# Optimization experiments

Measured on AMD Instinct MI355X. Metric: run time of the kernel, lower is better.

Reference implementation:

```python
import jax, jax.numpy as jnp
import numpy as np

B, T, C = 4, 2048, 1024
NH = 16
HD = C // NH  # 64


def setup_inputs() -> dict:
    key = jax.random.key(0)
    k1, k2, k3 = jax.random.split(key, 3)
    x = jax.random.normal(k1, (B, T, C), dtype=jnp.float32)
    # causal mask buffer, 1 = keep, 0 = mask out
    mask = jnp.tril(jnp.ones((T, T), dtype=jnp.int32))[None, None, :, :]
    # learned params (Linear with bias=False): torch stores weight as [out, in],
    # y = x @ W.T ; we store transposed for direct matmul
    w_qkv = jax.random.normal(k2, (C, 3 * C), dtype=jnp.float32) / np.sqrt(C)
    w_proj = jax.random.normal(k3, (C, C), dtype=jnp.float32) / np.sqrt(C)
    return {"x": x, "mask": mask, "w_qkv": w_qkv, "w_proj": w_proj}


def reference(x, mask, w_qkv, w_proj):
    b, t, c = x.shape
    qkv = x @ w_qkv  # [b, t, 3c]
    q, k, v = jnp.split(qkv, 3, axis=-1)
    # [b, nh, t, hd]
    q = q.reshape(b, t, NH, HD).transpose(0, 2, 1, 3)
    k = k.reshape(b, t, NH, HD).transpose(0, 2, 1, 3)
    v = v.reshape(b, t, NH, HD).transpose(0, 2, 1, 3)
    att = jnp.einsum("bhqd,bhkd->bhqk", q, k) * (1.0 / np.sqrt(HD))
    att = jnp.where(mask == 0, -jnp.inf, att)
    att = jax.nn.softmax(att, axis=-1)
    y = jnp.einsum("bhqk,bhkd->bhqd", att, v)
    y = y.transpose(0, 2, 1, 3).reshape(b, t, c)
    return y @ w_proj
```

## Files before the change

### kernel.cpp

```cpp
#include <hip/hip_runtime.h>
#include <hip/hip_bf16.h>

typedef _Float16 f16;
typedef __attribute__((ext_vector_type(4))) _Float16 f16x4;
typedef __attribute__((ext_vector_type(8))) _Float16 f16x8;
typedef __attribute__((ext_vector_type(4))) float f32x4;

#define MFMA16(a, b, c) __builtin_amdgcn_mfma_f32_16x16x16f16((a), (b), (c), 0, 0, 0)
#define MFMA32(a, b, c) __builtin_amdgcn_mfma_f32_16x16x32_f16((a), (b), (c), 0, 0, 0)
#define EXP2(x) __builtin_amdgcn_exp2f(x)
#define GLOAD_LDS16(g, l)                                                        \
  __builtin_amdgcn_global_load_lds((const __attribute__((address_space(1))) void*)(g), \
                                   (__attribute__((address_space(3))) void*)(l), 16, 0, 0)
typedef const __attribute__((address_space(3))) char* lds_cp;
#define TR16(dst, addr, imm) \
  asm volatile("ds_read_b64_tr_b16 %0, %1 offset:" imm : "=v"(dst) : "v"(addr))

__device__ __forceinline__ float max3f(float a, float b, float c) {
  return fmaxf(fmaxf(a, b), c);
}

__global__ __launch_bounds__(256) void prep_kernel(
    const float* __restrict__ x, f16* __restrict__ x16,
    const float* __restrict__ wq, f16* __restrict__ wqT,
    const float* __restrict__ wp, f16* __restrict__ wpT) {
  const int blk = blockIdx.x;
  const int tid = threadIdx.x;
  if (blk < 8192) {
    int i = blk * 256 + tid;
    const float4 v = reinterpret_cast<const float4*>(x)[i];
    f16x4 h;
    h[0] = (f16)v.x; h[1] = (f16)v.y; h[2] = (f16)v.z; h[3] = (f16)v.w;
    reinterpret_cast<f16x4*>(x16)[i] = h;
    return;
  }
  const float* src;
  f16* dst;
  int R, Cc, bx, by;
  if (blk < 11264) {
    int j = blk - 8192;
    bx = j % 96; by = j / 96;
    src = wq; dst = wqT; R = 1024; Cc = 3072;
  } else {
    int j = blk - 11264;
    bx = j & 31; by = j >> 5;
    src = wp; dst = wpT; R = 1024; Cc = 1024;
  }
  __shared__ float t[32][33];
  int tx0 = bx * 32, ty0 = by * 32;
  int c = tid & 31;
  int r0 = tid >> 5;
#pragma unroll
  for (int i = 0; i < 4; i++) {
    int r = r0 + 8 * i;
    t[r][c] = src[(size_t)(ty0 + r) * Cc + tx0 + c];
  }
  __syncthreads();
#pragma unroll
  for (int i = 0; i < 4; i++) {
    int a = r0 + 8 * i;
    dst[(size_t)(tx0 + a) * R + ty0 + c] = (f16)t[c][a];
  }
}

__global__ __launch_bounds__(512, 2) void gemm_qkv_kernel(
    const f16* __restrict__ A, const f16* __restrict__ Bt, f16* __restrict__ C,
    int M, int N, int K) {
  __shared__ __align__(16) char smem[114688];
  const int tid = threadIdx.x;
  const int lane = tid & 63, wid = tid >> 6;
  const int wm = wid >> 2, wn = wid & 3;
  const int lo = lane & 15, hi = lane >> 4;

  const int ntn = N / 192;
  const int nwg = (M >> 8) * ntn;
  const int wg = (blockIdx.x & 7) * (nwg >> 3) + (blockIdx.x >> 3);
  const int tm0 = (wg / ntn) << 8;
  const int tn0 = (wg % ntn) * 192;

  const int prow = tid >> 3;
  const int u8 = (tid & 7) ^ (prow & 7);
  const f16* asrc[4];
  const f16* bsrc[3];
#pragma unroll
  for (int c = 0; c < 4; c++) asrc[c] = A + (size_t)(tm0 + c * 64 + prow) * K + u8 * 8;
#pragma unroll
  for (int c = 0; c < 3; c++) bsrc[c] = Bt + (size_t)(tn0 + c * 64 + prow) * K + u8 * 8;

  const int swz = lo & 7;
  const int s0 = (hi ^ swz) << 4, s1 = ((4 + hi) ^ swz) << 4;
  const int aoff0 = wm * 16384 + lo * 128 + s0;
  const int aoff1 = wm * 16384 + lo * 128 + s1;
  int boff0[3], boff1[3];
#pragma unroll
  for (int ni = 0; ni < 3; ni++) {
    int cr = 3 * wn + ni;
    int base = 32768 + (cr >> 2) * 8192 + ((cr & 3) * 16 + lo) * 128;
    boff0[ni] = base + s0;
    boff1[ni] = base + s1;
  }

  f32x4 acc[8][3] = {};

  auto stageA = [&](int kt, char* buf) {
#pragma unroll
    for (int c = 0; c < 4; c++)
      GLOAD_LDS16(asrc[c] + kt, buf + c * 8192 + tid * 16);
  };
  auto stageB = [&](int kt, char* buf) {
#pragma unroll
    for (int c = 0; c < 3; c++)
      GLOAD_LDS16(bsrc[c] + kt, buf + 32768 + c * 8192 + tid * 16);
  };

  const int NT = K >> 6;
  stageA(0, smem);
  stageB(0, smem);

  for (int t = 0; t < NT; t++) {
    char* db = smem + (t & 1) * 57344;
    char* nb = smem + ((t + 1) & 1) * 57344;
    const int kt1 = (t + 1) << 6;

    asm volatile("s_waitcnt vmcnt(0)" ::: "memory");
    __builtin_amdgcn_s_barrier();
    f16x8 a[4][2], b[3][2];
#pragma unroll
    for (int mi = 0; mi < 4; mi++) {
      a[mi][0] = *(const f16x8*)(db + aoff0 + mi * 2048);
      a[mi][1] = *(const f16x8*)(db + aoff1 + mi * 2048);
    }
#pragma unroll
    for (int ni = 0; ni < 3; ni++) {
      b[ni][0] = *(const f16x8*)(db + boff0[ni]);
      b[ni][1] = *(const f16x8*)(db + boff1[ni]);
    }
    if (t + 1 < NT) stageA(kt1, nb);
    asm volatile("s_waitcnt lgkmcnt(0)" ::: "memory");
    __builtin_amdgcn_sched_barrier(0);
    __builtin_amdgcn_s_setprio(1);
#pragma unroll
    for (int mi = 0; mi < 4; mi++)
#pragma unroll
      for (int ni = 0; ni < 3; ni++) {
        acc[mi][ni] = MFMA32(a[mi][0], b[ni][0], acc[mi][ni]);
        acc[mi][ni] = MFMA32(a[mi][1], b[ni][1], acc[mi][ni]);
      }
    __builtin_amdgcn_s_setprio(0);

    __builtin_amdgcn_s_barrier();
#pragma unroll
    for (int mi = 0; mi < 4; mi++) {
      a[mi][0] = *(const f16x8*)(db + aoff0 + 8192 + mi * 2048);
      a[mi][1] = *(const f16x8*)(db + aoff1 + 8192 + mi * 2048);
    }
    if (t + 1 < NT) stageB(kt1, nb);
    asm volatile("s_waitcnt lgkmcnt(0)" ::: "memory");
    __builtin_amdgcn_sched_barrier(0);
    __builtin_amdgcn_s_setprio(1);
#pragma unroll
    for (int mi = 0; mi < 4; mi++)
#pragma unroll
      for (int ni = 0; ni < 3; ni++) {
        acc[4 + mi][ni] = MFMA32(a[mi][0], b[ni][0], acc[4 + mi][ni]);
        acc[4 + mi][ni] = MFMA32(a[mi][1], b[ni][1], acc[4 + mi][ni]);
      }
    __builtin_amdgcn_s_setprio(0);
  }

#pragma unroll
  for (int mi = 0; mi < 8; mi++)
#pragma unroll
    for (int ni = 0; ni < 3; ni++)
#pragma unroll
      for (int r = 0; r < 4; r++) {
        int row = tm0 + wm * 128 + mi * 16 + 4 * hi + r;
        int col = tn0 + wn * 48 + ni * 16 + lo;
        C[(size_t)row * N + col] = (f16)acc[mi][ni][r];
      }
}

template <bool OUT_F32>
__global__ __launch_bounds__(256) void gemm_f16_kernel(
    const f16* __restrict__ A, const f16* __restrict__ Bt, void* __restrict__ Cout,
    int M, int N, int K) {
  constexpr int BK = 32;
  __shared__ f16 Al[3][128 * BK];
  __shared__ f16 Bl[3][128 * BK];

  const int tid = threadIdx.x;
  const int lane = tid & 63, wid = tid >> 6;
  const int wm = wid >> 1, wn = wid & 1;
  const int lo = lane & 15, hi = lane >> 4;
  const int tn0 = blockIdx.x * 128, tm0 = blockIdx.y * 128;

  f32x4 acc[4][4] = {};

  const int r1 = tid >> 2, o1 = (tid & 3) * 8;

  auto stage = [&](int kt, int c) {
    GLOAD_LDS16(&A[(size_t)(tm0 + r1) * K + kt + o1], &Al[c][tid * 8]);
    GLOAD_LDS16(&A[(size_t)(tm0 + r1 + 64) * K + kt + o1], &Al[c][(tid + 256) * 8]);
    GLOAD_LDS16(&Bt[(size_t)(tn0 + r1) * K + kt + o1], &Bl[c][tid * 8]);
    GLOAD_LDS16(&Bt[(size_t)(tn0 + r1 + 64) * K + kt + o1], &Bl[c][(tid + 256) * 8]);
  };

  auto compute = [&](int cur) {
    f16x8 af[4], bf[4];
#pragma unroll
    for (int mi = 0; mi < 4; mi++)
      af[mi] = *(const f16x8*)&Al[cur][(wm * 64 + mi * 16 + lo) * BK + 8 * hi];
#pragma unroll
    for (int ni = 0; ni < 4; ni++)
      bf[ni] = *(const f16x8*)&Bl[cur][(wn * 64 + ni * 16 + lo) * BK + 8 * hi];
    __builtin_amdgcn_s_setprio(1);
#pragma unroll
    for (int mi = 0; mi < 4; mi++)
#pragma unroll
      for (int ni = 0; ni < 4; ni++)
        acc[mi][ni] = MFMA32(af[mi], bf[ni], acc[mi][ni]);
    __builtin_amdgcn_s_setprio(0);
  };

  const int NT = K / BK;
  stage(0, 0);
  stage(BK, 1);

  int cur = 0;
  for (int t = 0; t < NT - 1; t++) {
    asm volatile("s_waitcnt vmcnt(4)" ::: "memory");
    __builtin_amdgcn_s_barrier();
    if (t + 2 < NT) stage((t + 2) * BK, (t + 2) % 3);
    compute(cur);
    cur = (cur == 2) ? 0 : cur + 1;
  }
  asm volatile("s_waitcnt vmcnt(0)" ::: "memory");
  __builtin_amdgcn_s_barrier();
  compute(cur);

#pragma unroll
  for (int mi = 0; mi < 4; mi++)
#pragma unroll
    for (int ni = 0; ni < 4; ni++)
#pragma unroll
      for (int r = 0; r < 4; r++) {
        int row = tm0 + wm * 64 + mi * 16 + 4 * hi + r;
        int col = tn0 + wn * 64 + ni * 16 + lo;
        float v = acc[mi][ni][r];
        if (OUT_F32)
          ((float*)Cout)[(size_t)row * N + col] = v;
        else
          ((f16*)Cout)[(size_t)row * N + col] = (f16)v;
      }
}

__global__ __launch_bounds__(256, 4) void attn_kernel(
    const f16* __restrict__ qkv, f16* __restrict__ y) {
  constexpr int T = 2048, NHD = 3072, LDO = 72;
  const int bh = blockIdx.x;
  const int b = bh >> 4, h = bh & 15;
  const int pr = blockIdx.y;
  const int tid = threadIdx.x;
  const int lane = tid & 63, w = tid >> 6;
  const int lo = lane & 15, hi = lane >> 4;

  const size_t base = (size_t)b * T * NHD + (size_t)h * 64;
  const f16* Qp = qkv + base;
  const f16* Kp = qkv + base + 1024;
  const f16* Vp = qkv + base + 2048;

  __shared__ __align__(16) char smem[32768];
  f16 (*Ol)[LDO] = (f16(*)[LDO])smem;

  const int tile[2] = {pr, 31 - pr};
  const int qb[2] = {tile[0] * 64 + w * 16, tile[1] * 64 + w * 16};

  const float scf = 0.125f * 1.44269504089f;
  f16x8 qf[2][2];
#pragma unroll
  for (int s = 0; s < 2; s++) {
    const f16* qrow = Qp + (size_t)(qb[s] + lo) * NHD;
#pragma unroll
    for (int ks = 0; ks < 2; ks++) {
      f16x8 v = *(const f16x8*)&qrow[ks * 32 + 8 * hi];
#pragma unroll
      for (int j = 0; j < 8; j++) v[j] = (f16)((float)v[j] * scf);
      qf[s][ks] = v;
    }
  }

  f32x4 oacc[2][4] = {};
  f32x4 lacc[2] = {};
  float mreg[2] = {-1e30f, -1e30f};
  const f16x4 ones4 = {(f16)1.f, (f16)1.f, (f16)1.f, (f16)1.f};

  const int kr = tid >> 3;
  const int kslot = (tid & 7) ^ (kr & 7);
  const int tp = tid & 127;
  const int vkey = 4 * (tp >> 3) + ((tp >> 1) & 3);
  const int vcol = (tid >> 7) * 16 + (tid & 1) * 8;

  const int kfo0 = lo * 64 + ((hi ^ (lo & 7)) * 8);
  const int kfo1 = lo * 64 + (((4 + hi) ^ (lo & 7)) * 8);

  auto stage = [&](int kv, int c) {
    char* kb = smem + c * 8192;
    char* vb = smem + 16384 + c * 8192;
    GLOAD_LDS16(&Kp[(size_t)(kv + kr) * NHD + kslot * 8], kb + tid * 16);
    GLOAD_LDS16(&Kp[(size_t)(kv + kr + 32) * NHD + kslot * 8], kb + 4096 + tid * 16);
    GLOAD_LDS16(&Vp[(size_t)(kv + vkey) * NHD + vcol], vb + tid * 16);
    GLOAD_LDS16(&Vp[(size_t)(kv + vkey) * NHD + vcol + 32], vb + 4096 + tid * 16);
  };

  const int nt = 32 - pr;
  stage(0, 0);
  asm volatile("s_waitcnt vmcnt(0)" ::: "memory");
  __builtin_amdgcn_s_barrier();

  for (int t = 0; t < nt; t++) {
    const int cur = t & 1;
    const int kv0 = t * 64;
    if (t + 1 < nt) stage(kv0 + 64, cur ^ 1);

    const f16* Kl = (const f16*)(smem + cur * 8192);
    const bool act0 = kv0 <= qb[0] + 15;

    f16x8 kf[2][4];
#pragma unroll
    for (int ct = 0; ct < 4; ct++) {
      kf[0][ct] = *(const f16x8*)&Kl[ct * 1024 + kfo0];
      kf[1][ct] = *(const f16x8*)&Kl[ct * 1024 + kfo1];
    }

    f16x4 pb[2][4];
#pragma unroll
    for (int s = 0; s < 2; s++) {
      if (s == 0 && !act0) continue;
      f32x4 s_[4] = {};
      __builtin_amdgcn_s_setprio(1);
#pragma unroll
      for (int ks = 0; ks < 2; ks++)
#pragma unroll
        for (int ct = 0; ct < 4; ct++)
          s_[ct] = MFMA32(kf[ks][ct], qf[s][ks], s_[ct]);
      __builtin_amdgcn_s_setprio(0);

      if (kv0 + 63 > qb[s]) {
        const int q = qb[s] + lo;
#pragma unroll
        for (int ct = 0; ct < 4; ct++)
#pragma unroll
          for (int r = 0; r < 4; r++)
            if (kv0 + ct * 16 + 4 * hi + r > q) s_[ct][r] = -3.0e38f;
      }
      float t0 = max3f(s_[0][0], s_[0][1], s_[0][2]);
      float t1 = max3f(s_[0][3], s_[1][0], s_[1][1]);
      float t2 = max3f(s_[1][2], s_[1][3], s_[2][0]);
      float t3 = max3f(s_[2][1], s_[2][2], s_[2][3]);
      float t4 = max3f(s_[3][0], s_[3][1], s_[3][2]);
      float mt = fmaxf(max3f(t0, t1, t2), max3f(t3, t4, s_[3][3]));
      mt = fmaxf(mt, __shfl_xor(mt, 16));
      mt = fmaxf(mt, __shfl_xor(mt, 32));
      float mn = mreg[s];
      if (!__all(mt <= mn + 8.f)) {
        mn = fmaxf(mn, mt);
        const float al = EXP2(mreg[s] - mn);
        mreg[s] = mn;
#pragma unroll
        for (int r = 0; r < 4; r++) lacc[s][r] *= al;
#pragma unroll
        for (int ct = 0; ct < 4; ct++)
#pragma unroll
          for (int r = 0; r < 4; r++) oacc[s][ct][r] *= al;
      }
#pragma unroll
      for (int ct = 0; ct < 4; ct++)
#pragma unroll
        for (int r = 0; r < 4; r++)
          pb[s][ct][r] = (f16)EXP2(s_[ct][r] - mn);
      __builtin_amdgcn_s_setprio(1);
#pragma unroll
      for (int kk = 0; kk < 4; kk++)
        lacc[s] = MFMA16(ones4, pb[s][kk], lacc[s]);
      __builtin_amdgcn_s_setprio(0);
    }

    lds_cp vtrb = (lds_cp)(smem + 16384 + cur * 8192) + lane * 8;
#pragma unroll
    for (int ct = 0; ct < 4; ct++) {
      lds_cp bct = vtrb + ct * 2048;
      f16x4 v0, v1, v2, v3;
      TR16(v0, bct, "0");
      TR16(v1, bct, "512");
      TR16(v2, bct, "1024");
      TR16(v3, bct, "1536");
      asm volatile("s_waitcnt lgkmcnt(0)" ::: "memory");
      __builtin_amdgcn_sched_barrier(0);
      __builtin_amdgcn_s_setprio(1);
      if (act0) {
        oacc[0][ct] = MFMA16(v0, pb[0][0], oacc[0][ct]);
        oacc[0][ct] = MFMA16(v1, pb[0][1], oacc[0][ct]);
        oacc[0][ct] = MFMA16(v2, pb[0][2], oacc[0][ct]);
        oacc[0][ct] = MFMA16(v3, pb[0][3], oacc[0][ct]);
      }
      oacc[1][ct] = MFMA16(v0, pb[1][0], oacc[1][ct]);
      oacc[1][ct] = MFMA16(v1, pb[1][1], oacc[1][ct]);
      oacc[1][ct] = MFMA16(v2, pb[1][2], oacc[1][ct]);
      oacc[1][ct] = MFMA16(v3, pb[1][3], oacc[1][ct]);
      __builtin_amdgcn_s_setprio(0);
    }

    asm volatile("s_waitcnt vmcnt(0)" ::: "memory");
    __builtin_amdgcn_s_barrier();
  }

#pragma unroll
  for (int s = 0; s < 2; s++) {
    __syncthreads();
    const float inv = 1.f / lacc[s][0];
#pragma unroll
    for (int ct = 0; ct < 4; ct++) {
      f16x4 o4;
#pragma unroll
      for (int r = 0; r < 4; r++) o4[r] = (f16)(oacc[s][ct][r] * inv);
      *(f16x4*)&Ol[w * 16 + lo][ct * 16 + 4 * hi] = o4;
    }
    __syncthreads();
#pragma unroll
    for (int i = 0; i < 2; i++) {
      int idx = tid + 256 * i;
      int qq = idx >> 3, ch = idx & 7;
      *(f16x8*)&y[((size_t)b * T + tile[s] * 64 + qq) * 1024 + (size_t)h * 64 + ch * 8] =
          *(const f16x8*)&Ol[qq][ch * 8];
    }
  }
}

extern "C" void kernel_launch(void* const* d_in, const int* in_sizes, int n_in,
                              void* d_out, int out_size, void* d_ws, size_t ws_size,
                              hipStream_t stream) {
  const float* x = (const float*)d_in[0];
  const float* w_qkv = (const float*)d_in[2];
  const float* w_proj = (const float*)d_in[3];

  constexpr int B = 4, T = 2048, C = 1024, NH = 16;
  constexpr int M = B * T;
  constexpr int N1 = 3 * C;

  char* ws = (char*)d_ws;
  f16* x16 = (f16*)ws;    ws += (size_t)M * C * 2;
  f16* wqkvT = (f16*)ws;  ws += (size_t)N1 * C * 2;
  f16* wprojT = (f16*)ws; ws += (size_t)C * C * 2;
  f16* qkvb = (f16*)ws;   ws += (size_t)M * N1 * 2;
  f16* y16 = (f16*)ws;

  prep_kernel<<<12288, 256, 0, stream>>>(x, x16, w_qkv, wqkvT, w_proj, wprojT);
  gemm_qkv_kernel<<<(M / 256) * (N1 / 192), 512, 0, stream>>>(x16, wqkvT, qkvb, M, N1, C);
  attn_kernel<<<dim3(B * NH, 16), 256, 0, stream>>>(qkvb, y16);
  gemm_f16_kernel<true><<<dim3(C / 128, M / 128), 256, 0, stream>>>(y16, wprojT, (float*)d_out, M, C, C);
}
```

Baseline: 173.2 us.

## Unify GEMMs into a triple-buffered 256x128 kernel with deeper prefetch

Replaces the QKV GEMM (256x192 tile, double buffer, split-half staging) and the projection GEMM (128x128 tile, BK=32) with one templated kernel. It uses 256x128 tiles with BK=64, a three-stage LDS ring and prefetch two tiles ahead, waiting with vmcnt(6). The aim is better latency hiding and one barrier per k-step instead of two, and the projection GEMM gets the larger, swizzled tile. In exchange it needs 144KB of LDS per block, limiting occupancy to one block per CU, and the QKV tile becomes narrower.

```diff
diff --git a/kernel.cpp b/kernel.cpp
--- a/kernel.cpp
+++ b/kernel.cpp
@@ -63,189 +63,109 @@
   }
 }
 
-__global__ __launch_bounds__(512, 2) void gemm_qkv_kernel(
-    const f16* __restrict__ A, const f16* __restrict__ Bt, f16* __restrict__ C,
+template <bool OUT_F32>
+__global__ __launch_bounds__(512, 2) void gemm_deep_kernel(
+    const f16* __restrict__ A, const f16* __restrict__ Bt, void* __restrict__ Cout,
     int M, int N, int K) {
-  __shared__ __align__(16) char smem[114688];
+  __shared__ __align__(16) char smem[147456];
   const int tid = threadIdx.x;
   const int lane = tid & 63, wid = tid >> 6;
   const int wm = wid >> 2, wn = wid & 3;
   const int lo = lane & 15, hi = lane >> 4;
 
-  const int ntn = N / 192;
+  const int ntn = N >> 7;
   const int nwg = (M >> 8) * ntn;
   const int wg = (blockIdx.x & 7) * (nwg >> 3) + (blockIdx.x >> 3);
   const int tm0 = (wg / ntn) << 8;
-  const int tn0 = (wg % ntn) * 192;
+  const int tn0 = (wg % ntn) << 7;
 
   const int prow = tid >> 3;
   const int u8 = (tid & 7) ^ (prow & 7);
   const f16* asrc[4];
-  const f16* bsrc[3];
+  const f16* bsrc[2];
 #pragma unroll
   for (int c = 0; c < 4; c++) asrc[c] = A + (size_t)(tm0 + c * 64 + prow) * K + u8 * 8;
 #pragma unroll
-  for (int c = 0; c < 3; c++) bsrc[c] = Bt + (size_t)(tn0 + c * 64 + prow) * K + u8 * 8;
+  for (int c = 0; c < 2; c++) bsrc[c] = Bt + (size_t)(tn0 + c * 64 + prow) * K + u8 * 8;
 
   const int swz = lo & 7;
   const int s0 = (hi ^ swz) << 4, s1 = ((4 + hi) ^ swz) << 4;
-  const int aoff0 = wm * 16384 + lo * 128 + s0;
-  const int aoff1 = wm * 16384 + lo * 128 + s1;
-  int boff0[3], boff1[3];
-#pragma unroll
-  for (int ni = 0; ni < 3; ni++) {
-    int cr = 3 * wn + ni;
-    int base = 32768 + (cr >> 2) * 8192 + ((cr & 3) * 16 + lo) * 128;
+  const int abase0 = wm * 16384 + lo * 128 + s0;
+  const int abase1 = wm * 16384 + lo * 128 + s1;
+  int boff0[2], boff1[2];
+#pragma unroll
+  for (int ni = 0; ni < 2; ni++) {
+    int g = 2 * wn + ni;
+    int base = 32768 + (g >> 2) * 8192 + ((g & 3) * 16 + lo) * 128;
     boff0[ni] = base + s0;
     boff1[ni] = base + s1;
   }
 
-  f32x4 acc[8][3] = {};
-
-  auto stageA = [&](int kt, char* buf) {
+  f32x4 acc[8][2] = {};
+
+  auto stage = [&](int kt, char* buf) {
+    const int ke = kt << 6;
 #pragma unroll
     for (int c = 0; c < 4; c++)
-      GLOAD_LDS16(asrc[c] + kt, buf + c * 8192 + tid * 16);
+      GLOAD_LDS16(asrc[c] + ke, buf + c * 8192 + tid * 16);
+#pragma unroll
+    for (int c = 0; c < 2; c++)
+      GLOAD_LDS16(bsrc[c] + ke, buf + 32768 + c * 8192 + tid * 16);
   };
-  auto stageB = [&](int kt, char* buf) {
-#pragma unroll
-    for (int c = 0; c < 3; c++)
-      GLOAD_LDS16(bsrc[c] + kt, buf + 32768 + c * 8192 + tid * 16);
-  };
 
   const int NT = K >> 6;
-  stageA(0, smem);
-  stageB(0, smem);
-
+  stage(0, smem);
+  stage(1, smem + 49152);
+
+  int bufi = 0;
   for (int t = 0; t < NT; t++) {
-    char* db = smem + (t & 1) * 57344;
-    char* nb = smem + ((t + 1) & 1) * 57344;
-    const int kt1 = (t + 1) << 6;
-
-    asm volatile("s_waitcnt vmcnt(0)" ::: "memory");
+    char* db = smem + bufi * 49152;
+    if (t + 1 < NT) {
+      asm volatile("s_waitcnt vmcnt(6)" ::: "memory");
+    } else {
+      asm volatile("s_waitcnt vmcnt(0)" ::: "memory");
+    }
     __builtin_amdgcn_s_barrier();
-    f16x8 a[4][2], b[3][2];
-#pragma unroll
-    for (int mi = 0; mi < 4; mi++) {
-      a[mi][0] = *(const f16x8*)(db + aoff0 + mi * 2048);
-      a[mi][1] = *(const f16x8*)(db + aoff1 + mi * 2048);
-    }
-#pragma unroll
-    for (int ni = 0; ni < 3; ni++) {
+    if (t + 2 < NT) {
+      int nb = bufi + 2;
+      if (nb >= 3) nb -= 3;
+      stage(t + 2, smem + nb * 49152);
+    }
+    __builtin_amdgcn_sched_barrier(0);
+
+    f16x8 a[8][2], b[2][2];
+#pragma unroll
+    for (int mi = 0; mi < 8; mi++) {
+      int off = (mi >> 2) * 8192 + (mi & 3) * 2048;
+      a[mi][0] = *(const f16x8*)(db + abase0 + off);
+      a[mi][1] = *(const f16x8*)(db + abase1 + off);
+    }
+#pragma unroll
+    for (int ni = 0; ni < 2; ni++) {
       b[ni][0] = *(const f16x8*)(db + boff0[ni]);
       b[ni][1] = *(const f16x8*)(db + boff1[ni]);
     }
-    if (t + 1 < NT) stageA(kt1, nb);
-    asm volatile("s_waitcnt lgkmcnt(0)" ::: "memory");
-    __builtin_amdgcn_sched_barrier(0);
     __builtin_amdgcn_s_setprio(1);
 #pragma unroll
-    for (int mi = 0; mi < 4; mi++)
-#pragma unroll
-      for (int ni = 0; ni < 3; ni++) {
+    for (int mi = 0; mi < 8; mi++)
+#pragma unroll
+      for (int ni = 0; ni < 2; ni++) {
         acc[mi][ni] = MFMA32(a[mi][0], b[ni][0], acc[mi][ni]);
         acc[mi][ni] = MFMA32(a[mi][1], b[ni][1], acc[mi][ni]);
       }
     __builtin_amdgcn_s_setprio(0);
 
-    __builtin_amdgcn_s_barrier();
-#pragma unroll
-    for (int mi = 0; mi < 4; mi++) {
-      a[mi][0] = *(const f16x8*)(db + aoff0 + 8192 + mi * 2048);
-      a[mi][1] = *(const f16x8*)(db + aoff1 + 8192 + mi * 2048);
-    }
-    if (t + 1 < NT) stageB(kt1, nb);
-    asm volatile("s_waitcnt lgkmcnt(0)" ::: "memory");
-    __builtin_amdgcn_sched_barrier(0);
-    __builtin_amdgcn_s_setprio(1);
-#pragma unroll
-    for (int mi = 0; mi < 4; mi++)
-#pragma unroll
-      for (int ni = 0; ni < 3; ni++) {
-        acc[4 + mi][ni] = MFMA32(a[mi][0], b[ni][0], acc[4 + mi][ni]);
-        acc[4 + mi][ni] = MFMA32(a[mi][1], b[ni][1], acc[4 + mi][ni]);
-      }
-    __builtin_amdgcn_s_setprio(0);
+    bufi = (bufi == 2) ? 0 : bufi + 1;
   }
 
 #pragma unroll
   for (int mi = 0; mi < 8; mi++)
 #pragma unroll
-    for (int ni = 0; ni < 3; ni++)
+    for (int ni = 0; ni < 2; ni++)
 #pragma unroll
       for (int r = 0; r < 4; r++) {
         int row = tm0 + wm * 128 + mi * 16 + 4 * hi + r;
-        int col = tn0 + wn * 48 + ni * 16 + lo;
-        C[(size_t)row * N + col] = (f16)acc[mi][ni][r];
-      }
-}
-
-template <bool OUT_F32>
-__global__ __launch_bounds__(256) void gemm_f16_kernel(
-    const f16* __restrict__ A, const f16* __restrict__ Bt, void* __restrict__ Cout,
-    int M, int N, int K) {
-  constexpr int BK = 32;
-  __shared__ f16 Al[3][128 * BK];
-  __shared__ f16 Bl[3][128 * BK];
-
-  const int tid = threadIdx.x;
-  const int lane = tid & 63, wid = tid >> 6;
-  const int wm = wid >> 1, wn = wid & 1;
-  const int lo = lane & 15, hi = lane >> 4;
-  const int tn0 = blockIdx.x * 128, tm0 = blockIdx.y * 128;
-
-  f32x4 acc[4][4] = {};
-
-  const int r1 = tid >> 2, o1 = (tid & 3) * 8;
-
-  auto stage = [&](int kt, int c) {
-    GLOAD_LDS16(&A[(size_t)(tm0 + r1) * K + kt + o1], &Al[c][tid * 8]);
-    GLOAD_LDS16(&A[(size_t)(tm0 + r1 + 64) * K + kt + o1], &Al[c][(tid + 256) * 8]);
-    GLOAD_LDS16(&Bt[(size_t)(tn0 + r1) * K + kt + o1], &Bl[c][tid * 8]);
-    GLOAD_LDS16(&Bt[(size_t)(tn0 + r1 + 64) * K + kt + o1], &Bl[c][(tid + 256) * 8]);
-  };
-
-  auto compute = [&](int cur) {
-    f16x8 af[4], bf[4];
-#pragma unroll
-    for (int mi = 0; mi < 4; mi++)
-      af[mi] = *(const f16x8*)&Al[cur][(wm * 64 + mi * 16 + lo) * BK + 8 * hi];
-#pragma unroll
-    for (int ni = 0; ni < 4; ni++)
-      bf[ni] = *(const f16x8*)&Bl[cur][(wn * 64 + ni * 16 + lo) * BK + 8 * hi];
-    __builtin_amdgcn_s_setprio(1);
-#pragma unroll
-    for (int mi = 0; mi < 4; mi++)
-#pragma unroll
-      for (int ni = 0; ni < 4; ni++)
-        acc[mi][ni] = MFMA32(af[mi], bf[ni], acc[mi][ni]);
-    __builtin_amdgcn_s_setprio(0);
-  };
-
-  const int NT = K / BK;
-  stage(0, 0);
-  stage(BK, 1);
-
-  int cur = 0;
-  for (int t = 0; t < NT - 1; t++) {
-    asm volatile("s_waitcnt vmcnt(4)" ::: "memory");
-    __builtin_amdgcn_s_barrier();
-    if (t + 2 < NT) stage((t + 2) * BK, (t + 2) % 3);
-    compute(cur);
-    cur = (cur == 2) ? 0 : cur + 1;
-  }
-  asm volatile("s_waitcnt vmcnt(0)" ::: "memory");
-  __builtin_amdgcn_s_barrier();
-  compute(cur);
-
-#pragma unroll
-  for (int mi = 0; mi < 4; mi++)
-#pragma unroll
-    for (int ni = 0; ni < 4; ni++)
-#pragma unroll
-      for (int r = 0; r < 4; r++) {
-        int row = tm0 + wm * 64 + mi * 16 + 4 * hi + r;
-        int col = tn0 + wn * 64 + ni * 16 + lo;
+        int col = tn0 + wn * 32 + ni * 16 + lo;
         float v = acc[mi][ni][r];
         if (OUT_F32)
           ((float*)Cout)[(size_t)row * N + col] = v;
@@ -455,7 +375,7 @@
   f16* y16 = (f16*)ws;
 
   prep_kernel<<<12288, 256, 0, stream>>>(x, x16, w_qkv, wqkvT, w_proj, wprojT);
-  gemm_qkv_kernel<<<(M / 256) * (N1 / 192), 512, 0, stream>>>(x16, wqkvT, qkvb, M, N1, C);
+  gemm_deep_kernel<false><<<(M / 256) * (N1 / 128), 512, 0, stream>>>(x16, wqkvT, qkvb, M, N1, C);
   attn_kernel<<<dim3(B * NH, 16), 256, 0, stream>>>(qkvb, y16);
-  gemm_f16_kernel<true><<<dim3(C / 128, M / 128), 256, 0, stream>>>(y16, wprojT, (float*)d_out, M, C, C);
-}
+  gemm_deep_kernel<true><<<(M / 256) * (C / 128), 512, 0, stream>>>(y16, wprojT, (float*)d_out, M, C, C);
+}
```

New measurement: 172.6 us. About the same (-0.3%).
